# Performance work log

Hardware: AMD Instinct MI355X
Metric: run time of the kernel (lower is better)

The kernel has to match this reference:

```python
import jax, jax.numpy as jnp
import numpy as np

B, DZ = 65536, 512

def setup_inputs() -> dict:
    key = jax.random.key(0)
    k1, k2, k3 = jax.random.split(key, 3)
    r = 1.0 / np.sqrt(DZ)
    z = jax.random.normal(k1, (B, DZ), dtype=jnp.float32)
    AW = jax.random.uniform(k2, (DZ, DZ), dtype=jnp.float32, minval=-r, maxval=r)
    h = jax.random.uniform(k3, (DZ,), dtype=jnp.float32, minval=-r, maxval=r)
    return {"z": z, "AW": AW, "h": h}

def reference(z, AW, h):
    # split AW into diagonal (A) and off-diagonal (W) parts
    A = jnp.diag(AW)                     # [dz]
    W = AW - jnp.diag(A)                 # [dz, dz], zero diagonal
    # mean-subtraction layer norm + ReLU
    z_act = jax.nn.relu(z - jnp.mean(z, axis=-1, keepdims=True))  # [B, dz]
    # z_new = A*z + z_act @ W^T + h
    return A * z + z_act @ W.T + h
```

## Files before the change

### kernel.cpp

```cpp
#include <hip/hip_runtime.h>
#include <hip/hip_bf16.h>


#define DZV 512
#define BM 32
#define LDA 520

typedef __attribute__((ext_vector_type(8))) short short8;
typedef __attribute__((ext_vector_type(4))) float f32x4;

__device__ __forceinline__ unsigned short f2bf(float x) {
  __hip_bfloat16 b = __float2bfloat16(x);
  return __builtin_bit_cast(unsigned short, b);
}
__device__ __forceinline__ float bf2f(unsigned short u) {
  return __builtin_bit_cast(float, (unsigned int)u << 16);
}

__global__ void pack_b(const float* __restrict__ AW, unsigned short* __restrict__ AWp,
                       float* __restrict__ Adiag) {
  int idx = blockIdx.x * 256 + threadIdx.x;
  int L = idx & 63, s = (idx >> 6) & 15, T = idx >> 10;
  int n = T * 16 + (L & 15);
  int k = s * 32 + (L >> 4) * 8;
  const float4* src = (const float4*)(AW + n * DZV + k);
  float4 a = src[0], b = src[1];
  union { unsigned short u[8]; short8 v; } p;
  p.u[0] = f2bf(a.x); p.u[1] = f2bf(a.y); p.u[2] = f2bf(a.z); p.u[3] = f2bf(a.w);
  p.u[4] = f2bf(b.x); p.u[5] = f2bf(b.y); p.u[6] = f2bf(b.z); p.u[7] = f2bf(b.w);
  *(short8*)(AWp + idx * 8) = p.v;
  if (idx < DZV) Adiag[idx] = AW[idx * (DZV + 1)];
}

__global__ __launch_bounds__(512, 4) void plrnn_step(
    const float* __restrict__ z, const float* __restrict__ h,
    const unsigned short* __restrict__ AWp, const float* __restrict__ Adiag,
    float* __restrict__ out)
{
  __shared__ unsigned short sA[BM * LDA];
  __shared__ unsigned short sC[BM * LDA];

  const int t = threadIdx.x;
  const int row0 = blockIdx.x * BM;

  const int lane = t & 63;
  const int wave = t >> 6;
  const int lr   = lane & 15;
  const int quad = lane >> 4;
  const int nbase = wave * 64;

  const unsigned short* bb[4];
  #pragma unroll
  for (int nt = 0; nt < 4; ++nt)
    bb[nt] = AWp + (((wave * 4 + nt) * 16) * 64 + lane) * 8;

  {
    const int r = t >> 4;
    const int c = t & 15;
    const float4* zr = (const float4*)(z + (row0 + r) * DZV);
    float4 v[8];
    float s = 0.f;
    #pragma unroll
    for (int i = 0; i < 8; ++i) {
      v[i] = zr[c + i * 16];
      s += (v[i].x + v[i].y) + (v[i].z + v[i].w);
    }
    s += __shfl_xor(s, 1);
    s += __shfl_xor(s, 2);
    s += __shfl_xor(s, 4);
    s += __shfl_xor(s, 8);
    const float mu = s * (1.0f / 512.0f);
    #pragma unroll
    for (int i = 0; i < 8; ++i) {
      const int c4 = c + i * 16;
      float4 Ad = ((const float4*)Adiag)[c4];
      float4 hv = ((const float4*)h)[c4];
      union { unsigned short u[4]; } pa, pc;
      pa.u[0] = f2bf(fmaxf(v[i].x - mu, 0.f));
      pa.u[1] = f2bf(fmaxf(v[i].y - mu, 0.f));
      pa.u[2] = f2bf(fmaxf(v[i].z - mu, 0.f));
      pa.u[3] = f2bf(fmaxf(v[i].w - mu, 0.f));
      pc.u[0] = f2bf(Ad.x * fminf(v[i].x, mu) + hv.x);
      pc.u[1] = f2bf(Ad.y * fminf(v[i].y, mu) + hv.y);
      pc.u[2] = f2bf(Ad.z * fminf(v[i].z, mu) + hv.z);
      pc.u[3] = f2bf(Ad.w * fminf(v[i].w, mu) + hv.w);
      *(ushort4*)&sA[r * LDA + c4 * 4] = *(ushort4*)pa.u;
      *(ushort4*)&sC[r * LDA + c4 * 4] = *(ushort4*)pc.u;
    }
  }

  short8 bf[2][4];
  #pragma unroll
  for (int nt = 0; nt < 4; ++nt)
    bf[0][nt] = *(const short8*)(bb[nt] + 0 * 512);

  __syncthreads();

  const unsigned short* a0 = &sA[(lr) * LDA + quad * 8];
  const unsigned short* a1 = &sA[(16 + lr) * LDA + quad * 8];

  short8 af[2][2];
  af[0][0] = *(const short8*)(a0);
  af[0][1] = *(const short8*)(a1);

  f32x4 acc[2][4];
  #pragma unroll
  for (int mt = 0; mt < 2; ++mt)
    #pragma unroll
    for (int nt = 0; nt < 4; ++nt)
      acc[mt][nt] = (f32x4){0.f, 0.f, 0.f, 0.f};

  #pragma unroll
  for (int s = 0; s < 16; ++s) {
    const int cur = s & 1, nxt = cur ^ 1;
    if (s < 15) {
      #pragma unroll
      for (int nt = 0; nt < 4; ++nt)
        bf[nxt][nt] = *(const short8*)(bb[nt] + (s + 1) * 512);
      af[nxt][0] = *(const short8*)(a0 + (s + 1) * 32);
      af[nxt][1] = *(const short8*)(a1 + (s + 1) * 32);
    }
    #pragma unroll
    for (int nt = 0; nt < 4; ++nt) {
      acc[0][nt] = __builtin_amdgcn_mfma_f32_16x16x32_bf16(af[cur][0], bf[cur][nt], acc[0][nt], 0, 0, 0);
      acc[1][nt] = __builtin_amdgcn_mfma_f32_16x16x32_bf16(af[cur][1], bf[cur][nt], acc[1][nt], 0, 0, 0);
    }
  }

  #pragma unroll
  for (int mt = 0; mt < 2; ++mt) {
    #pragma unroll
    for (int r = 0; r < 4; ++r) {
      const int lm = mt * 16 + quad * 4 + r;
      float corr[4];
      #pragma unroll
      for (int nt = 0; nt < 4; ++nt)
        corr[nt] = bf2f(sC[lm * LDA + nbase + nt * 16 + lr]);
      float* orow = out + (row0 + lm) * DZV + nbase + lr;
      #pragma unroll
      for (int nt = 0; nt < 4; ++nt)
        orow[nt * 16] = acc[mt][nt][r] + corr[nt];
    }
  }
}

extern "C" void kernel_launch(void* const* d_in, const int* in_sizes, int n_in,
                              void* d_out, int out_size, void* d_ws, size_t ws_size,
                              hipStream_t stream) {
  const float* z  = (const float*)d_in[0];
  const float* AW = (const float*)d_in[1];
  const float* h  = (const float*)d_in[2];
  float* out = (float*)d_out;
  unsigned short* AWp = (unsigned short*)d_ws;
  float* Adiag = (float*)((char*)d_ws + DZV * DZV * sizeof(unsigned short));

  pack_b<<<128, 256, 0, stream>>>(AW, AWp, Adiag);
  plrnn_step<<<65536 / BM, 512, 0, stream>>>(z, h, AWp, Adiag, out);
}
```

Baseline: 265.4 us.

## Double row tile to 64, drop correction LDS buffer, recompute epilogue from z

Raises the row tile from 32 to 64 so each block reuses every loaded B fragment across four M-tiles, which halves global B traffic per row. The bf16 correction buffer in LDS is removed; the epilogue instead re-reads z from global/L2 with per-row means kept in LDS and computes A*min(z,mu)+h in fp32. Output is written with nontemporal stores. In exchange, z is read twice, register pressure rises with 16 accumulators, and the A-fragment software prefetch from LDS is dropped.

```diff
diff --git a/kernel.cpp b/kernel.cpp
--- a/kernel.cpp
+++ b/kernel.cpp
@@ -3,7 +3,7 @@
 
 
 #define DZV 512
-#define BM 32
+#define BM 64
 #define LDA 520
 
 typedef __attribute__((ext_vector_type(8))) short short8;
@@ -12,9 +12,6 @@
 __device__ __forceinline__ unsigned short f2bf(float x) {
   __hip_bfloat16 b = __float2bfloat16(x);
   return __builtin_bit_cast(unsigned short, b);
-}
-__device__ __forceinline__ float bf2f(unsigned short u) {
-  return __builtin_bit_cast(float, (unsigned int)u << 16);
 }
 
 __global__ void pack_b(const float* __restrict__ AW, unsigned short* __restrict__ AWp,
@@ -38,7 +35,7 @@
     float* __restrict__ out)
 {
   __shared__ unsigned short sA[BM * LDA];
-  __shared__ unsigned short sC[BM * LDA];
+  __shared__ float sMu[BM];
 
   const int t = threadIdx.x;
   const int row0 = blockIdx.x * BM;
@@ -55,91 +52,94 @@
     bb[nt] = AWp + (((wave * 4 + nt) * 16) * 64 + lane) * 8;
 
   {
-    const int r = t >> 4;
+    const int rr = t >> 4;
     const int c = t & 15;
-    const float4* zr = (const float4*)(z + (row0 + r) * DZV);
-    float4 v[8];
-    float s = 0.f;
     #pragma unroll
-    for (int i = 0; i < 8; ++i) {
-      v[i] = zr[c + i * 16];
-      s += (v[i].x + v[i].y) + (v[i].z + v[i].w);
-    }
-    s += __shfl_xor(s, 1);
-    s += __shfl_xor(s, 2);
-    s += __shfl_xor(s, 4);
-    s += __shfl_xor(s, 8);
-    const float mu = s * (1.0f / 512.0f);
-    #pragma unroll
-    for (int i = 0; i < 8; ++i) {
-      const int c4 = c + i * 16;
-      float4 Ad = ((const float4*)Adiag)[c4];
-      float4 hv = ((const float4*)h)[c4];
-      union { unsigned short u[4]; } pa, pc;
-      pa.u[0] = f2bf(fmaxf(v[i].x - mu, 0.f));
-      pa.u[1] = f2bf(fmaxf(v[i].y - mu, 0.f));
-      pa.u[2] = f2bf(fmaxf(v[i].z - mu, 0.f));
-      pa.u[3] = f2bf(fmaxf(v[i].w - mu, 0.f));
-      pc.u[0] = f2bf(Ad.x * fminf(v[i].x, mu) + hv.x);
-      pc.u[1] = f2bf(Ad.y * fminf(v[i].y, mu) + hv.y);
-      pc.u[2] = f2bf(Ad.z * fminf(v[i].z, mu) + hv.z);
-      pc.u[3] = f2bf(Ad.w * fminf(v[i].w, mu) + hv.w);
-      *(ushort4*)&sA[r * LDA + c4 * 4] = *(ushort4*)pa.u;
-      *(ushort4*)&sC[r * LDA + c4 * 4] = *(ushort4*)pc.u;
+    for (int p = 0; p < 2; ++p) {
+      const int r = p * 32 + rr;
+      const float4* zr = (const float4*)(z + (row0 + r) * DZV);
+      float4 v[8];
+      float s = 0.f;
+      #pragma unroll
+      for (int i = 0; i < 8; ++i) {
+        v[i] = zr[c + i * 16];
+        s += (v[i].x + v[i].y) + (v[i].z + v[i].w);
+      }
+      s += __shfl_xor(s, 1);
+      s += __shfl_xor(s, 2);
+      s += __shfl_xor(s, 4);
+      s += __shfl_xor(s, 8);
+      const float mu = s * (1.0f / 512.0f);
+      if (c == 0) sMu[r] = mu;
+      #pragma unroll
+      for (int i = 0; i < 8; ++i) {
+        const int c4 = c + i * 16;
+        union { unsigned short u[4]; ushort4 v4; } pa;
+        pa.u[0] = f2bf(fmaxf(v[i].x - mu, 0.f));
+        pa.u[1] = f2bf(fmaxf(v[i].y - mu, 0.f));
+        pa.u[2] = f2bf(fmaxf(v[i].z - mu, 0.f));
+        pa.u[3] = f2bf(fmaxf(v[i].w - mu, 0.f));
+        *(ushort4*)&sA[r * LDA + c4 * 4] = pa.v4;
+      }
     }
   }
 
   short8 bf[2][4];
   #pragma unroll
   for (int nt = 0; nt < 4; ++nt)
-    bf[0][nt] = *(const short8*)(bb[nt] + 0 * 512);
+    bf[0][nt] = *(const short8*)(bb[nt]);
 
   __syncthreads();
 
-  const unsigned short* a0 = &sA[(lr) * LDA + quad * 8];
-  const unsigned short* a1 = &sA[(16 + lr) * LDA + quad * 8];
+  const unsigned short* abase = &sA[lr * LDA + quad * 8];
 
-  short8 af[2][2];
-  af[0][0] = *(const short8*)(a0);
-  af[0][1] = *(const short8*)(a1);
-
-  f32x4 acc[2][4];
+  f32x4 acc[4][4];
   #pragma unroll
-  for (int mt = 0; mt < 2; ++mt)
+  for (int mt = 0; mt < 4; ++mt)
     #pragma unroll
     for (int nt = 0; nt < 4; ++nt)
       acc[mt][nt] = (f32x4){0.f, 0.f, 0.f, 0.f};
 
+  short8 af[4];
   #pragma unroll
   for (int s = 0; s < 16; ++s) {
     const int cur = s & 1, nxt = cur ^ 1;
+    #pragma unroll
+    for (int mt = 0; mt < 4; ++mt)
+      af[mt] = *(const short8*)(abase + mt * 16 * LDA + s * 32);
     if (s < 15) {
       #pragma unroll
       for (int nt = 0; nt < 4; ++nt)
         bf[nxt][nt] = *(const short8*)(bb[nt] + (s + 1) * 512);
-      af[nxt][0] = *(const short8*)(a0 + (s + 1) * 32);
-      af[nxt][1] = *(const short8*)(a1 + (s + 1) * 32);
     }
     #pragma unroll
-    for (int nt = 0; nt < 4; ++nt) {
-      acc[0][nt] = __builtin_amdgcn_mfma_f32_16x16x32_bf16(af[cur][0], bf[cur][nt], acc[0][nt], 0, 0, 0);
-      acc[1][nt] = __builtin_amdgcn_mfma_f32_16x16x32_bf16(af[cur][1], bf[cur][nt], acc[1][nt], 0, 0, 0);
-    }
+    for (int nt = 0; nt < 4; ++nt)
+      #pragma unroll
+      for (int mt = 0; mt < 4; ++mt)
+        acc[mt][nt] = __builtin_amdgcn_mfma_f32_16x16x32_bf16(af[mt], bf[cur][nt], acc[mt][nt], 0, 0, 0);
   }
 
+  float Ad[4], hv[4];
   #pragma unroll
-  for (int mt = 0; mt < 2; ++mt) {
+  for (int nt = 0; nt < 4; ++nt) {
+    const int col = nbase + nt * 16 + lr;
+    Ad[nt] = Adiag[col];
+    hv[nt] = h[col];
+  }
+  #pragma unroll
+  for (int mt = 0; mt < 4; ++mt) {
     #pragma unroll
     for (int r = 0; r < 4; ++r) {
       const int lm = mt * 16 + quad * 4 + r;
-      float corr[4];
-      #pragma unroll
-      for (int nt = 0; nt < 4; ++nt)
-        corr[nt] = bf2f(sC[lm * LDA + nbase + nt * 16 + lr]);
+      const float mu = sMu[lm];
+      const float* zrow = z + (row0 + lm) * DZV + nbase + lr;
       float* orow = out + (row0 + lm) * DZV + nbase + lr;
       #pragma unroll
-      for (int nt = 0; nt < 4; ++nt)
-        orow[nt * 16] = acc[mt][nt][r] + corr[nt];
+      for (int nt = 0; nt < 4; ++nt) {
+        const float zv = zrow[nt * 16];
+        const float corr = Ad[nt] * fminf(zv, mu) + hv[nt];
+        __builtin_nontemporal_store(acc[mt][nt][r] + corr, &orow[nt * 16]);
+      }
     }
   }
 }
```

Measured after the change: 323.2 us. 21.7% more time.

## Make plrnn_step persistent with double-buffered LDS and prefetch of next z tile

Applied to the files above, without the earlier changes.

Replaces the launch of 2048 one-tile blocks with 256 persistent blocks, each processing 8 row tiles. The sA/sC LDS buffers are double-buffered, and the next tile's z rows are loaded into registers while the current tile's MFMA loop runs. This aims to hide global-load latency and cut block launch overhead. In exchange, LDS per block doubles, occupancy drops to 2 blocks per CU, and a 256-block grid may underfill the GPU's CUs.

```diff
diff --git a/kernel.cpp b/kernel.cpp
--- a/kernel.cpp
+++ b/kernel.cpp
@@ -5,6 +5,8 @@
 #define DZV 512
 #define BM 32
 #define LDA 520
+#define NBLK 256
+#define NTILE 8
 
 typedef __attribute__((ext_vector_type(8))) short short8;
 typedef __attribute__((ext_vector_type(4))) float f32x4;
@@ -32,39 +34,35 @@
   if (idx < DZV) Adiag[idx] = AW[idx * (DZV + 1)];
 }
 
-__global__ __launch_bounds__(512, 4) void plrnn_step(
+__global__ __launch_bounds__(512, 2) void plrnn_step(
     const float* __restrict__ z, const float* __restrict__ h,
     const unsigned short* __restrict__ AWp, const float* __restrict__ Adiag,
     float* __restrict__ out)
 {
-  __shared__ unsigned short sA[BM * LDA];
-  __shared__ unsigned short sC[BM * LDA];
+  __shared__ unsigned short sA[2][BM * LDA];
+  __shared__ unsigned short sC[2][BM * LDA];
 
   const int t = threadIdx.x;
-  const int row0 = blockIdx.x * BM;
-
   const int lane = t & 63;
   const int wave = t >> 6;
   const int lr   = lane & 15;
   const int quad = lane >> 4;
   const int nbase = wave * 64;
+  const int rr = t >> 4;
+  const int c  = t & 15;
 
   const unsigned short* bb[4];
   #pragma unroll
   for (int nt = 0; nt < 4; ++nt)
     bb[nt] = AWp + (((wave * 4 + nt) * 16) * 64 + lane) * 8;
 
-  {
-    const int r = t >> 4;
-    const int c = t & 15;
-    const float4* zr = (const float4*)(z + (row0 + r) * DZV);
-    float4 v[8];
+  float4 v[8];
+
+  auto phase1 = [&](int buf) {
     float s = 0.f;
     #pragma unroll
-    for (int i = 0; i < 8; ++i) {
-      v[i] = zr[c + i * 16];
+    for (int i = 0; i < 8; ++i)
       s += (v[i].x + v[i].y) + (v[i].z + v[i].w);
-    }
     s += __shfl_xor(s, 1);
     s += __shfl_xor(s, 2);
     s += __shfl_xor(s, 4);
@@ -75,7 +73,7 @@
       const int c4 = c + i * 16;
       float4 Ad = ((const float4*)Adiag)[c4];
       float4 hv = ((const float4*)h)[c4];
-      union { unsigned short u[4]; } pa, pc;
+      union { unsigned short u[4]; ushort4 v4; } pa, pc;
       pa.u[0] = f2bf(fmaxf(v[i].x - mu, 0.f));
       pa.u[1] = f2bf(fmaxf(v[i].y - mu, 0.f));
       pa.u[2] = f2bf(fmaxf(v[i].z - mu, 0.f));
@@ -84,62 +82,83 @@
       pc.u[1] = f2bf(Ad.y * fminf(v[i].y, mu) + hv.y);
       pc.u[2] = f2bf(Ad.z * fminf(v[i].z, mu) + hv.z);
       pc.u[3] = f2bf(Ad.w * fminf(v[i].w, mu) + hv.w);
-      *(ushort4*)&sA[r * LDA + c4 * 4] = *(ushort4*)pa.u;
-      *(ushort4*)&sC[r * LDA + c4 * 4] = *(ushort4*)pc.u;
+      *(ushort4*)&sA[buf][rr * LDA + c4 * 4] = pa.v4;
+      *(ushort4*)&sC[buf][rr * LDA + c4 * 4] = pc.v4;
     }
+  };
+
+  {
+    const float4* zr = (const float4*)(z + ((long)blockIdx.x * BM + rr) * DZV);
+    #pragma unroll
+    for (int i = 0; i < 8; ++i) v[i] = zr[c + i * 16];
   }
+  phase1(0);
 
   short8 bf[2][4];
   #pragma unroll
   for (int nt = 0; nt < 4; ++nt)
-    bf[0][nt] = *(const short8*)(bb[nt] + 0 * 512);
-
+    bf[0][nt] = *(const short8*)(bb[nt]);
   __syncthreads();
 
-  const unsigned short* a0 = &sA[(lr) * LDA + quad * 8];
-  const unsigned short* a1 = &sA[(16 + lr) * LDA + quad * 8];
+  #pragma unroll 1
+  for (int k = 0; k < NTILE; ++k) {
+    const int cur = k & 1;
+    const int row0 = (blockIdx.x + k * NBLK) * BM;
 
-  short8 af[2][2];
-  af[0][0] = *(const short8*)(a0);
-  af[0][1] = *(const short8*)(a1);
+    if (k + 1 < NTILE) {
+      const float4* zr =
+          (const float4*)(z + ((long)(blockIdx.x + (k + 1) * NBLK) * BM + rr) * DZV);
+      #pragma unroll
+      for (int i = 0; i < 8; ++i) v[i] = zr[c + i * 16];
+    }
 
-  f32x4 acc[2][4];
-  #pragma unroll
-  for (int mt = 0; mt < 2; ++mt)
+    const unsigned short* abase = &sA[cur][lr * LDA + quad * 8];
+    f32x4 acc[2][4];
     #pragma unroll
-    for (int nt = 0; nt < 4; ++nt)
-      acc[mt][nt] = (f32x4){0.f, 0.f, 0.f, 0.f};
-
-  #pragma unroll
-  for (int s = 0; s < 16; ++s) {
-    const int cur = s & 1, nxt = cur ^ 1;
-    if (s < 15) {
+    for (int mt = 0; mt < 2; ++mt)
       #pragma unroll
       for (int nt = 0; nt < 4; ++nt)
-        bf[nxt][nt] = *(const short8*)(bb[nt] + (s + 1) * 512);
-      af[nxt][0] = *(const short8*)(a0 + (s + 1) * 32);
-      af[nxt][1] = *(const short8*)(a1 + (s + 1) * 32);
+        acc[mt][nt] = (f32x4){0.f, 0.f, 0.f, 0.f};
+
+    #pragma unroll
+    for (int s = 0; s < 16; ++s) {
+      const int cs = s & 1, ns = cs ^ 1;
+      short8 af0 = *(const short8*)(abase + s * 32);
+      short8 af1 = *(const short8*)(abase + 16 * LDA + s * 32);
+      if (s < 15) {
+        #pragma unroll
+        for (int nt = 0; nt < 4; ++nt)
+          bf[ns][nt] = *(const short8*)(bb[nt] + (s + 1) * 512);
+      }
+      #pragma unroll
+      for (int nt = 0; nt < 4; ++nt) {
+        acc[0][nt] = __builtin_amdgcn_mfma_f32_16x16x32_bf16(af0, bf[cs][nt], acc[0][nt], 0, 0, 0);
+        acc[1][nt] = __builtin_amdgcn_mfma_f32_16x16x32_bf16(af1, bf[cs][nt], acc[1][nt], 0, 0, 0);
+      }
     }
+
     #pragma unroll
-    for (int nt = 0; nt < 4; ++nt) {
-      acc[0][nt] = __builtin_amdgcn_mfma_f32_16x16x32_bf16(af[cur][0], bf[cur][nt], acc[0][nt], 0, 0, 0);
-      acc[1][nt] = __builtin_amdgcn_mfma_f32_16x16x32_bf16(af[cur][1], bf[cur][nt], acc[1][nt], 0, 0, 0);
+    for (int mt = 0; mt < 2; ++mt) {
+      #pragma unroll
+      for (int r = 0; r < 4; ++r) {
+        const int lm = mt * 16 + quad * 4 + r;
+        float corr[4];
+        #pragma unroll
+        for (int nt = 0; nt < 4; ++nt)
+          corr[nt] = bf2f(sC[cur][lm * LDA + nbase + nt * 16 + lr]);
+        float* orow = out + (long)(row0 + lm) * DZV + nbase + lr;
+        #pragma unroll
+        for (int nt = 0; nt < 4; ++nt)
+          orow[nt * 16] = acc[mt][nt][r] + corr[nt];
+      }
     }
-  }
 
-  #pragma unroll
-  for (int mt = 0; mt < 2; ++mt) {
-    #pragma unroll
-    for (int r = 0; r < 4; ++r) {
-      const int lm = mt * 16 + quad * 4 + r;
-      float corr[4];
+    if (k + 1 < NTILE) {
+      phase1(cur ^ 1);
       #pragma unroll
       for (int nt = 0; nt < 4; ++nt)
-        corr[nt] = bf2f(sC[lm * LDA + nbase + nt * 16 + lr]);
-      float* orow = out + (row0 + lm) * DZV + nbase + lr;
-      #pragma unroll
-      for (int nt = 0; nt < 4; ++nt)
-        orow[nt * 16] = acc[mt][nt][r] + corr[nt];
+        bf[0][nt] = *(const short8*)(bb[nt]);
+      __syncthreads();
     }
   }
 }
@@ -155,5 +174,5 @@
   float* Adiag = (float*)((char*)d_ws + DZV * DZV * sizeof(unsigned short));
 
   pack_b<<<128, 256, 0, stream>>>(AW, AWp, Adiag);
-  plrnn_step<<<65536 / BM, 512, 0, stream>>>(z, h, AWp, Adiag, out);
+  plrnn_step<<<NBLK, 512, 0, stream>>>(z, h, AWp, Adiag, out);
 }
```

New measurement: 347.9 us. 31.1% more time.

## Warp-specialize into producer and consumer waves with double-buffered persistent tiles

Applied to the files above, without the earlier changes.

The kernel becomes persistent: 256 blocks of 1024 threads, each working through 8 row tiles. Eight producer waves load z, compute the mean, ReLU and correction terms, and write bf16 tiles into double-buffered LDS. Eight consumer waves run the MFMA GEMM and the epilogue on the previous tile, with a barrier at each step. The goal is to overlap global loads of z with matrix compute. In exchange it doubles LDS use, halves the waves doing MFMA, and may lower occupancy; the grid of 256 blocks may also underfill the GPU.

```diff
diff --git a/kernel.cpp b/kernel.cpp
--- a/kernel.cpp
+++ b/kernel.cpp
@@ -5,6 +5,8 @@
 #define DZV 512
 #define BM 32
 #define LDA 520
+#define TPB 8
+#define NBLK 256
 
 typedef __attribute__((ext_vector_type(8))) short short8;
 typedef __attribute__((ext_vector_type(4))) float f32x4;
@@ -32,115 +34,125 @@
   if (idx < DZV) Adiag[idx] = AW[idx * (DZV + 1)];
 }
 
-__global__ __launch_bounds__(512, 4) void plrnn_step(
+__global__ __launch_bounds__(1024, 4) void plrnn_step(
     const float* __restrict__ z, const float* __restrict__ h,
     const unsigned short* __restrict__ AWp, const float* __restrict__ Adiag,
     float* __restrict__ out)
 {
-  __shared__ unsigned short sA[BM * LDA];
-  __shared__ unsigned short sC[BM * LDA];
+  __shared__ unsigned short sA[2][BM * LDA];
+  __shared__ unsigned short sC[2][BM * LDA];
 
   const int t = threadIdx.x;
-  const int row0 = blockIdx.x * BM;
-
   const int lane = t & 63;
   const int wave = t >> 6;
-  const int lr   = lane & 15;
+  const bool prod = wave < 8;
+  const long tile0 = (long)blockIdx.x * TPB;
+
+  const int cw = wave & 7;
+  const int lr = lane & 15;
   const int quad = lane >> 4;
-  const int nbase = wave * 64;
-
+  const int nbase = cw * 64;
   const unsigned short* bb[4];
   #pragma unroll
   for (int nt = 0; nt < 4; ++nt)
-    bb[nt] = AWp + (((wave * 4 + nt) * 16) * 64 + lane) * 8;
+    bb[nt] = AWp + (((cw * 4 + nt) * 16) * 64 + lane) * 8;
 
-  {
-    const int r = t >> 4;
-    const int c = t & 15;
-    const float4* zr = (const float4*)(z + (row0 + r) * DZV);
-    float4 v[8];
-    float s = 0.f;
+  short8 bf[2][4];
+  if (!prod) {
     #pragma unroll
-    for (int i = 0; i < 8; ++i) {
-      v[i] = zr[c + i * 16];
-      s += (v[i].x + v[i].y) + (v[i].z + v[i].w);
-    }
-    s += __shfl_xor(s, 1);
-    s += __shfl_xor(s, 2);
-    s += __shfl_xor(s, 4);
-    s += __shfl_xor(s, 8);
-    const float mu = s * (1.0f / 512.0f);
-    #pragma unroll
-    for (int i = 0; i < 8; ++i) {
-      const int c4 = c + i * 16;
-      float4 Ad = ((const float4*)Adiag)[c4];
-      float4 hv = ((const float4*)h)[c4];
-      union { unsigned short u[4]; } pa, pc;
-      pa.u[0] = f2bf(fmaxf(v[i].x - mu, 0.f));
-      pa.u[1] = f2bf(fmaxf(v[i].y - mu, 0.f));
-      pa.u[2] = f2bf(fmaxf(v[i].z - mu, 0.f));
-      pa.u[3] = f2bf(fmaxf(v[i].w - mu, 0.f));
-      pc.u[0] = f2bf(Ad.x * fminf(v[i].x, mu) + hv.x);
-      pc.u[1] = f2bf(Ad.y * fminf(v[i].y, mu) + hv.y);
-      pc.u[2] = f2bf(Ad.z * fminf(v[i].z, mu) + hv.z);
-      pc.u[3] = f2bf(Ad.w * fminf(v[i].w, mu) + hv.w);
-      *(ushort4*)&sA[r * LDA + c4 * 4] = *(ushort4*)pa.u;
-      *(ushort4*)&sC[r * LDA + c4 * 4] = *(ushort4*)pc.u;
-    }
+    for (int nt = 0; nt < 4; ++nt)
+      bf[0][nt] = *(const short8*)(bb[nt]);
   }
 
-  short8 bf[2][4];
-  #pragma unroll
-  for (int nt = 0; nt < 4; ++nt)
-    bf[0][nt] = *(const short8*)(bb[nt] + 0 * 512);
+  const int prow = (wave & 7) * 4 + (lane >> 4);
+  const int pc = lane & 15;
 
-  __syncthreads();
+  for (int j = 0; j <= TPB; ++j) {
+    if (prod) {
+      if (j < TPB) {
+        const int buf = j & 1;
+        const float4* zr = (const float4*)(z + ((tile0 + j) * BM + prow) * (long)DZV);
+        float4 v[8];
+        float s = 0.f;
+        #pragma unroll
+        for (int i = 0; i < 8; ++i) {
+          v[i] = zr[pc + i * 16];
+          s += (v[i].x + v[i].y) + (v[i].z + v[i].w);
+        }
+        s += __shfl_xor(s, 1);
+        s += __shfl_xor(s, 2);
+        s += __shfl_xor(s, 4);
+        s += __shfl_xor(s, 8);
+        const float mu = s * (1.0f / 512.0f);
+        #pragma unroll
+        for (int i = 0; i < 8; ++i) {
+          const int c4 = pc + i * 16;
+          float4 Ad = ((const float4*)Adiag)[c4];
+          float4 hv = ((const float4*)h)[c4];
+          union { unsigned short u[4]; ushort4 v4; } pa, pk;
+          pa.u[0] = f2bf(fmaxf(v[i].x - mu, 0.f));
+          pa.u[1] = f2bf(fmaxf(v[i].y - mu, 0.f));
+          pa.u[2] = f2bf(fmaxf(v[i].z - mu, 0.f));
+          pa.u[3] = f2bf(fmaxf(v[i].w - mu, 0.f));
+          pk.u[0] = f2bf(Ad.x * fminf(v[i].x, mu) + hv.x);
+          pk.u[1] = f2bf(Ad.y * fminf(v[i].y, mu) + hv.y);
+          pk.u[2] = f2bf(Ad.z * fminf(v[i].z, mu) + hv.z);
+          pk.u[3] = f2bf(Ad.w * fminf(v[i].w, mu) + hv.w);
+          *(ushort4*)&sA[buf][prow * LDA + c4 * 4] = pa.v4;
+          *(ushort4*)&sC[buf][prow * LDA + c4 * 4] = pk.v4;
+        }
+      }
+    } else {
+      if (j >= 1) {
+        const int buf = (j - 1) & 1;
+        const long row0 = (tile0 + (j - 1)) * BM;
+        const unsigned short* a0 = &sA[buf][lr * LDA + quad * 8];
+        const unsigned short* a1 = a0 + 16 * LDA;
+        short8 af[2][2];
+        af[0][0] = *(const short8*)(a0);
+        af[0][1] = *(const short8*)(a1);
+        f32x4 acc[2][4];
+        #pragma unroll
+        for (int mt = 0; mt < 2; ++mt)
+          #pragma unroll
+          for (int nt = 0; nt < 4; ++nt)
+            acc[mt][nt] = (f32x4){0.f, 0.f, 0.f, 0.f};
 
-  const unsigned short* a0 = &sA[(lr) * LDA + quad * 8];
-  const unsigned short* a1 = &sA[(16 + lr) * LDA + quad * 8];
+        #pragma unroll
+        for (int s = 0; s < 16; ++s) {
+          const int cur = s & 1, nxt = cur ^ 1;
+          #pragma unroll
+          for (int nt = 0; nt < 4; ++nt)
+            bf[nxt][nt] = *(const short8*)(bb[nt] + ((s + 1) & 15) * 512);
+          if (s < 15) {
+            af[nxt][0] = *(const short8*)(a0 + (s + 1) * 32);
+            af[nxt][1] = *(const short8*)(a1 + (s + 1) * 32);
+          }
+          #pragma unroll
+          for (int nt = 0; nt < 4; ++nt) {
+            acc[0][nt] = __builtin_amdgcn_mfma_f32_16x16x32_bf16(af[cur][0], bf[cur][nt], acc[0][nt], 0, 0, 0);
+            acc[1][nt] = __builtin_amdgcn_mfma_f32_16x16x32_bf16(af[cur][1], bf[cur][nt], acc[1][nt], 0, 0, 0);
+          }
+        }
 
-  short8 af[2][2];
-  af[0][0] = *(const short8*)(a0);
-  af[0][1] = *(const short8*)(a1);
-
-  f32x4 acc[2][4];
-  #pragma unroll
-  for (int mt = 0; mt < 2; ++mt)
-    #pragma unroll
-    for (int nt = 0; nt < 4; ++nt)
-      acc[mt][nt] = (f32x4){0.f, 0.f, 0.f, 0.f};
-
-  #pragma unroll
-  for (int s = 0; s < 16; ++s) {
-    const int cur = s & 1, nxt = cur ^ 1;
-    if (s < 15) {
-      #pragma unroll
-      for (int nt = 0; nt < 4; ++nt)
-        bf[nxt][nt] = *(const short8*)(bb[nt] + (s + 1) * 512);
-      af[nxt][0] = *(const short8*)(a0 + (s + 1) * 32);
-      af[nxt][1] = *(const short8*)(a1 + (s + 1) * 32);
+        #pragma unroll
+        for (int mt = 0; mt < 2; ++mt) {
+          #pragma unroll
+          for (int r = 0; r < 4; ++r) {
+            const int lm = mt * 16 + quad * 4 + r;
+            float corr[4];
+            #pragma unroll
+            for (int nt = 0; nt < 4; ++nt)
+              corr[nt] = bf2f(sC[buf][lm * LDA + nbase + nt * 16 + lr]);
+            float* orow = out + (row0 + lm) * (long)DZV + nbase + lr;
+            #pragma unroll
+            for (int nt = 0; nt < 4; ++nt)
+              orow[nt * 16] = acc[mt][nt][r] + corr[nt];
+          }
+        }
+      }
     }
-    #pragma unroll
-    for (int nt = 0; nt < 4; ++nt) {
-      acc[0][nt] = __builtin_amdgcn_mfma_f32_16x16x32_bf16(af[cur][0], bf[cur][nt], acc[0][nt], 0, 0, 0);
-      acc[1][nt] = __builtin_amdgcn_mfma_f32_16x16x32_bf16(af[cur][1], bf[cur][nt], acc[1][nt], 0, 0, 0);
-    }
-  }
-
-  #pragma unroll
-  for (int mt = 0; mt < 2; ++mt) {
-    #pragma unroll
-    for (int r = 0; r < 4; ++r) {
-      const int lm = mt * 16 + quad * 4 + r;
-      float corr[4];
-      #pragma unroll
-      for (int nt = 0; nt < 4; ++nt)
-        corr[nt] = bf2f(sC[lm * LDA + nbase + nt * 16 + lr]);
-      float* orow = out + (row0 + lm) * DZV + nbase + lr;
-      #pragma unroll
-      for (int nt = 0; nt < 4; ++nt)
-        orow[nt * 16] = acc[mt][nt][r] + corr[nt];
-    }
+    asm volatile("s_waitcnt lgkmcnt(0)\n\ts_barrier" ::: "memory");
   }
 }
 
@@ -155,5 +167,5 @@
   float* Adiag = (float*)((char*)d_ws + DZV * DZV * sizeof(unsigned short));
 
   pack_b<<<128, 256, 0, stream>>>(AW, AWp, Adiag);
-  plrnn_step<<<65536 / BM, 512, 0, stream>>>(z, h, AWp, Adiag, out);
+  plrnn_step<<<NBLK, 1024, 0, stream>>>(z, h, AWp, Adiag, out);
 }
```

After: 438.2 us. 1.65x slower.
